# Performance work log

Measured on AMD Instinct MI355X. Metric: run time of the kernel, lower is better.

Reference implementation:

```python
import jax, jax.numpy as jnp
import numpy as np


def _gcn_conv(x, W, b, src, dst, num_nodes):
    # PyG GCNConv: h = x @ W; symmetric normalization with self-loops; scatter-add; + bias
    h = x @ W
    deg = jax.ops.segment_sum(jnp.ones_like(dst, dtype=h.dtype), dst, num_segments=num_nodes)
    dinv = jnp.where(deg > 0, jax.lax.rsqrt(deg), 0.0)
    norm = dinv[src] * dinv[dst]                         # [E]
    msgs = h[src] * norm[:, None]                        # [E, H] gather + scale
    out = jax.ops.segment_sum(msgs, dst, num_segments=num_nodes)
    return out + b


def setup_inputs() -> dict:
    key = jax.random.key(0)
    ks = jax.random.split(key, 10)
    N, E = 500000, 1000000
    IN, H, SIG = 3, 64, 24
    x = jax.random.uniform(ks[0], (N, IN), dtype=jnp.float32)
    edge_index = jax.random.randint(ks[1], (2, E), 0, N, dtype=jnp.int64)
    batch = jnp.zeros((N,), dtype=jnp.int64)
    def glorot(k, shape):
        lim = np.sqrt(6.0 / (shape[0] + shape[1]))
        return jax.random.uniform(k, shape, dtype=jnp.float32, minval=-lim, maxval=lim)
    return {
        "x": x,
        "edge_index": edge_index,
        "batch": batch,
        "W1": glorot(ks[2], (IN, H)), "b1": jnp.zeros((H,), jnp.float32),
        "W2": glorot(ks[3], (H, H)),  "b2": jnp.zeros((H,), jnp.float32),
        "W3": glorot(ks[4], (H, H)),  "b3": jnp.zeros((H,), jnp.float32),
        "Wfc": glorot(ks[5], (H, SIG)), "bfc": jnp.zeros((SIG,), jnp.float32),
    }


def reference(x, edge_index, batch, W1, b1, W2, b2, W3, b3, Wfc, bfc):
    N = x.shape[0]
    NUM_GRAPHS = 1  # batch is all zeros (single graph)
    # add self-loops once (GCNConv adds them per layer; identical edge set each layer)
    loop = jnp.arange(N, dtype=edge_index.dtype)
    src = jnp.concatenate([edge_index[0], loop])
    dst = jnp.concatenate([edge_index[1], loop])

    h = jax.nn.relu(_gcn_conv(x, W1, b1, src, dst, N))
    h = jax.nn.relu(_gcn_conv(h, W2, b2, src, dst, N))
    h = jax.nn.relu(_gcn_conv(h, W3, b3, src, dst, N))

    # global mean pool per graph
    sums = jax.ops.segment_sum(h, batch, num_segments=NUM_GRAPHS)          # [G, H]
    counts = jax.ops.segment_sum(jnp.ones((N,), h.dtype), batch, num_segments=NUM_GRAPHS)
    sig = sums / jnp.maximum(counts, 1.0)[:, None]

    return jnp.tanh(sig @ Wfc + bfc)  # [G, 24]
```

## Files before the change

kernel.cpp:

```cpp
#include <hip/hip_runtime.h>
#include <hip/hip_bf16.h>
#include <hip/hip_fp16.h>


#define ALIGN256(x) (((x) + 255) & ~(size_t)255)
#define NBUCK_MAX 512

typedef _Float16 half8 __attribute__((ext_vector_type(8)));
typedef _Float16 half4 __attribute__((ext_vector_type(4)));
typedef float f32x4 __attribute__((ext_vector_type(4)));
typedef int i32x4 __attribute__((ext_vector_type(4)));

__device__ __forceinline__ void dec16(i32x4 r, half8& a, half8& b) {
    i32x4 u, v;
    u.x = (int)(((unsigned)r.x << 8) & 0xFF00FF00u);
    u.y = (int)(((unsigned)r.x)      & 0xFF00FF00u);
    u.z = (int)(((unsigned)r.y << 8) & 0xFF00FF00u);
    u.w = (int)(((unsigned)r.y)      & 0xFF00FF00u);
    v.x = (int)(((unsigned)r.z << 8) & 0xFF00FF00u);
    v.y = (int)(((unsigned)r.z)      & 0xFF00FF00u);
    v.z = (int)(((unsigned)r.w << 8) & 0xFF00FF00u);
    v.w = (int)(((unsigned)r.w)      & 0xFF00FF00u);
    a = *(half8*)&u; b = *(half8*)&v;
}

__device__ __forceinline__ unsigned char enc8(float x) {
    unsigned short hb = __half_as_ushort(__float2half(x));
    return (unsigned char)((hb + 0x80u) >> 8);
}

__global__ __launch_bounds__(256) void init_kernel(float* __restrict__ pool, half4* __restrict__ xs,
                                                   unsigned char* __restrict__ h8a,
                                                   unsigned char* __restrict__ h8b, int N) {
    int i = threadIdx.x;
    if (i < 64) pool[i] = 0.f;
    if (i < 16) {
        ((int*)(h8a + (size_t)N * 64))[i] = 0;
        ((int*)(h8b + (size_t)N * 64))[i] = 0;
    }
    if (i == 0) *(int2*)&xs[N] = make_int2(0, 0);
}

__global__ __launch_bounds__(256) void hist_kernel(const int* __restrict__ ei, int E, int CE, int SH,
                                                   int* __restrict__ cnt_mat) {
    __shared__ int h[NBUCK_MAX];
    const int t = threadIdx.x, blk = blockIdx.x;
    for (int i = t; i < NBUCK_MAX; i += 256) h[i] = 0;
    __syncthreads();
    const int e0 = blk * CE, e1 = min(E, e0 + CE);
    for (int e = e0 + t; e < e1; e += 256)
        atomicAdd(&h[ei[E + e] >> SH], 1);
    __syncthreads();
    for (int i = t; i < NBUCK_MAX; i += 256) cnt_mat[blk * NBUCK_MAX + i] = h[i];
}

__global__ __launch_bounds__(64) void colscan_kernel(const int* __restrict__ cnt_mat,
                                                     int* __restrict__ base_mat,
                                                     int* __restrict__ tot, int nblk) {
    __shared__ int ls[64];
    const int j = blockIdx.x;
    const int t = threadIdx.x;
    const int PER = (nblk + 63) >> 6;
    const int b0 = t * PER, b1 = min(nblk, b0 + PER);
    int s = 0;
    for (int b = b0; b < b1; ++b) s += cnt_mat[b * NBUCK_MAX + j];
    ls[t] = s;
    __syncthreads();
    if (t == 0) {
        int run = 0;
        for (int k = 0; k < 64; ++k) { int v = ls[k]; ls[k] = run; run += v; }
        tot[j] = run;
    }
    __syncthreads();
    int run = ls[t];
    for (int b = b0; b < b1; ++b) {
        int v = cnt_mat[b * NBUCK_MAX + j];
        base_mat[b * NBUCK_MAX + j] = run;
        run += v;
    }
}

__global__ __launch_bounds__(256) void totscan_kernel(const int* __restrict__ tot,
                                                      int* __restrict__ start, int NBK) {
    __shared__ int ls[256];
    const int t = threadIdx.x;
    const int PER = (NBK + 255) >> 8;
    const int j0 = t * PER, j1 = min(NBK, j0 + PER);
    int s = 0;
    for (int j = j0; j < j1; ++j) s += tot[j];
    ls[t] = s;
    __syncthreads();
    if (t == 0) {
        int run = 0;
        for (int k = 0; k < 256; ++k) { int v = ls[k]; ls[k] = run; run += v; }
    }
    __syncthreads();
    int run = ls[t];
    for (int j = j0; j < j1; ++j) { start[j] = run; run += tot[j]; }
}

__global__ __launch_bounds__(256) void scatter_kernel(const int* __restrict__ ei, int E, int CE, int SH,
                                                      const int* __restrict__ base_mat,
                                                      const int* __restrict__ start,
                                                      unsigned* __restrict__ bkt) {
    __shared__ int sbuf[4096];
    __shared__ unsigned short sb[4096];
    __shared__ int lh[NBUCK_MAX];
    __shared__ int lbase[NBUCK_MAX];
    __shared__ int cur[NBUCK_MAX];
    __shared__ int ls[256];
    const int t = threadIdx.x, blk = blockIdx.x;
    for (int i = t; i < NBUCK_MAX; i += 256) { lh[i] = 0; cur[i] = 0; }
    __syncthreads();
    const int e0 = blk * CE, e1 = min(E, e0 + CE);
    for (int e = e0 + t; e < e1; e += 256)
        atomicAdd(&lh[ei[E + e] >> SH], 1);
    __syncthreads();
    int a0 = lh[2 * t], a1 = lh[2 * t + 1];
    ls[t] = a0 + a1;
    __syncthreads();
    if (t == 0) {
        int run = 0;
        for (int k = 0; k < 256; ++k) { int v = ls[k]; ls[k] = run; run += v; }
    }
    __syncthreads();
    lbase[2 * t]     = ls[t];
    lbase[2 * t + 1] = ls[t] + a0;
    __syncthreads();
    const unsigned lowm = (1u << SH) - 1u;
    for (int e = e0 + t; e < e1; e += 256) {
        int s = ei[e], d = ei[E + e];
        int b = d >> SH;
        int r = atomicAdd(&cur[b], 1);
        int slot = lbase[b] + r;
        sbuf[slot] = (int)((((unsigned)d & lowm) << 21) | (unsigned)s);
        sb[slot] = (unsigned short)b;
    }
    __syncthreads();
    const int n = e1 - e0;
    for (int i = t; i < n; i += 256) {
        int b = sb[i];
        int dest = start[b] + base_mat[blk * NBUCK_MAX + b] + (i - lbase[b]);
        bkt[dest] = (unsigned)sbuf[i];
    }
}

__global__ __launch_bounds__(256) void build_kernel(const unsigned* __restrict__ bkt,
                                                    const int* __restrict__ start, const int* __restrict__ tot,
                                                    int SH, int nrows,
                                                    int* __restrict__ ell, int* __restrict__ sec) {
    __shared__ __align__(16) int loc[2048][8];
    const int t = threadIdx.x, j = blockIdx.x;
    const int R = 1 << SH;
    int4 z = make_int4(0, 0, 0, 0);
    for (int i = t; i < R * 2; i += 256) ((int4*)loc)[i] = z;
    __syncthreads();
    const int s0 = start[j], s1 = s0 + tot[j];
    for (int e = s0 + t; e < s1; e += 256) {
        unsigned p = bkt[e];
        int dl = (int)(p >> 21);
        int src = (int)(p & 0x1FFFFFu);
        int k = atomicAdd(&loc[dl][0], 1);
        if (k < 7) loc[dl][1 + k] = src;
        else if (k < 15) {
            int grow = (j << SH) + dl;
            sec[(size_t)grow * 8 + (k - 7)] = src;
        }
    }
    __syncthreads();
    const int base = j << SH;
    for (int i = t; i < R; i += 256) {
        int grow = base + i;
        if (grow < nrows) {
            int4* dst = (int4*)(ell + (size_t)grow * 8);
            dst[0] = ((int4*)&loc[i][0])[0];
            dst[1] = ((int4*)&loc[i][0])[1];
        }
    }
}

__global__ __launch_bounds__(256) void xs_kernel(const int* __restrict__ ell, const float* __restrict__ x,
                                                 half4* __restrict__ xs, int N) {
    int i = blockIdx.x * 256 + threadIdx.x;
    if (i < N) {
        float d = rsqrtf((float)(ell[(size_t)i * 8] + 1));
        half4 v;
        v[0] = (_Float16)(d * x[(size_t)i * 3 + 0]);
        v[1] = (_Float16)(d * x[(size_t)i * 3 + 1]);
        v[2] = (_Float16)(d * x[(size_t)i * 3 + 2]);
        v[3] = (_Float16)0.f;
        xs[i] = v;
    }
}

__global__ __launch_bounds__(256) void layer1_kernel(const half4* __restrict__ xs,
                                                     const int* __restrict__ ell,
                                                     const int* __restrict__ sec,
                                                     const float* __restrict__ W1, const float* __restrict__ b1,
                                                     unsigned char* __restrict__ hout, int N) {
    __shared__ float4 a1S[256];
    const int t = threadIdx.x;
    const int jg = blockIdx.x * 256 + t;
    const bool valid = (jg < N);
    const int jc = valid ? jg : N;

    half4 sv = xs[jc];
    float sx = (float)sv[0], sy = (float)sv[1], sz = (float)sv[2];
    const int* row = ell + (size_t)(valid ? jg : 0) * 8;
    int4 e0 = *(const int4*)row;
    int4 e1 = *(const int4*)(row + 4);
    int craw = valid ? e0.x : 0;
    int deg = min(craw, 15);
    int i0 = (deg > 0) ? e0.y : N;
    int i1 = (deg > 1) ? e0.z : N;
    int i2 = (deg > 2) ? e0.w : N;
    int i3 = (deg > 3) ? e1.x : N;
    int i4 = (deg > 4) ? e1.y : N;
    int i5 = (deg > 5) ? e1.z : N;
    int i6 = (deg > 6) ? e1.w : N;
    half4 q0 = xs[i0], q1 = xs[i1], q2 = xs[i2], q3 = xs[i3];
    half4 q4 = xs[i4], q5 = xs[i5], q6 = xs[i6];
    sx += (float)q0[0] + (float)q1[0] + (float)q2[0] + (float)q3[0]
        + (float)q4[0] + (float)q5[0] + (float)q6[0];
    sy += (float)q0[1] + (float)q1[1] + (float)q2[1] + (float)q3[1]
        + (float)q4[1] + (float)q5[1] + (float)q6[1];
    sz += (float)q0[2] + (float)q1[2] + (float)q2[2] + (float)q3[2]
        + (float)q4[2] + (float)q5[2] + (float)q6[2];
    if (deg > 7) {
        const int* srow = sec + (size_t)jg * 8;
        for (int i = 7; i < deg; ++i) {
            half4 qq = xs[srow[i - 7]];
            sx += (float)qq[0]; sy += (float)qq[1]; sz += (float)qq[2];
        }
    }
    float dj = valid ? rsqrtf((float)(craw + 1)) : 0.f;
    a1S[t] = make_float4(dj * sx, dj * sy, dj * sz, dj);
    __syncthreads();

    const int l = t & 63, w = t >> 6;
    const float w0 = W1[l], w1 = W1[64 + l], w2 = W1[128 + l], bl = b1[l];
    const int base = blockIdx.x * 256 + w * 64;
    #pragma unroll 4
    for (int n = 0; n < 64; ++n) {
        int j2 = base + n;
        if (j2 >= N) break;
        float4 a = a1S[w * 64 + n];
        float v = fmaf(a.x, w0, fmaf(a.y, w1, fmaf(a.z, w2, bl)));
        hout[(size_t)j2 * 64 + l] = enc8(a.w * fmaxf(v, 0.f));
    }
}

template <int POOL>
__global__ __launch_bounds__(256) void layer_kernel(const unsigned char* __restrict__ hin,
                                                    const int* __restrict__ ell,
                                                    const int* __restrict__ sec,
                                                    const float* __restrict__ W, const float* __restrict__ bias,
                                                    unsigned char* __restrict__ hout, float* __restrict__ pool, int N) {
    const int t = threadIdx.x;
    const int l = t & 63;
    const int w = t >> 6;
    const int l15 = l & 15, q = l >> 4;
    const int m = l >> 2, qq = l & 3;
    const int cbase = l & ~3;

    __shared__ float red[256];
    __shared__ __align__(16) _Float16 wlds[8 * 64 * 8];
    __shared__ __align__(16) int tbuf[4][16 * 36];

    for (int c = t; c < 512; c += 256) {
        int f = c >> 6, ln = c & 63;
        int ct = f >> 1, kt = f & 1;
        int q2 = ln >> 4, m2 = ln & 15;
        half8 b;
        #pragma unroll
        for (int j = 0; j < 8; ++j) {
            int g = 4 * q2 + (j >> 1);
            int ii = g & 7, blk = g >> 3;
            int feat = 16 * blk + 4 * (ii >> 1) + (ii & 1) + 2 * (j & 1);
            b[j] = (_Float16)W[(kt * 32 + feat) * 64 + ct * 16 + m2];
        }
        *(half8*)&wlds[(size_t)c * 8] = b;
    }
    float bb[4];
    #pragma unroll
    for (int ct = 0; ct < 4; ++ct) bb[ct] = bias[ct * 16 + l15];
    __syncthreads();

    const char* hb = (const char*)hin;
    const int vlo = qq * 16;
    float ps0 = 0.f, ps1 = 0.f, ps2 = 0.f, ps3 = 0.f;

    const int ngroups = (N + 15) >> 4;
    const int gstride = gridDim.x * 4;
    for (int g = blockIdx.x * 4 + w; g < ngroups; g += gstride) {
        const int j0 = g << 4;
        const int jm = j0 + m;
        const bool validm = (jm < N);
        const int jsm = validm ? jm : N;

        i32x4 iv = *(const i32x4*)(ell + (size_t)jsm * 8 + (qq & 1) * 4);

        int cnt = __shfl(iv.x, cbase, 64);
        int s1  = __shfl(iv.y, cbase, 64);
        int s2  = __shfl(iv.z, cbase, 64);
        int s3  = __shfl(iv.w, cbase, 64);
        int s4  = __shfl(iv.x, cbase + 1, 64);
        int s5  = __shfl(iv.y, cbase + 1, 64);
        int s6  = __shfl(iv.z, cbase + 1, 64);
        int s7  = __shfl(iv.w, cbase + 1, 64);

        int craw = validm ? cnt : 0;
        int degc = min(craw, 15);
        float djv = rsqrtf((float)(craw + 1));

        int dmax = degc;
        dmax = max(dmax, __shfl_xor(dmax, 4, 64));
        dmax = max(dmax, __shfl_xor(dmax, 8, 64));
        dmax = max(dmax, __shfl_xor(dmax, 16, 64));
        dmax = max(dmax, __shfl_xor(dmax, 32, 64));

        s1 = (degc > 0) ? s1 : N;
        s2 = (degc > 1) ? s2 : N;
        s3 = (degc > 2) ? s3 : N;
        s4 = (degc > 3) ? s4 : N;
        s5 = (degc > 4) ? s5 : N;
        s6 = (degc > 5) ? s6 : N;
        s7 = (degc > 6) ? s7 : N;

        i32x4 rS = *(const i32x4*)(hb + ((size_t)jsm << 6) + vlo);
        i32x4 r1 = *(const i32x4*)(hb + ((size_t)(unsigned)s1 << 6) + vlo);
        i32x4 r2 = *(const i32x4*)(hb + ((size_t)(unsigned)s2 << 6) + vlo);
        i32x4 r3 = *(const i32x4*)(hb + ((size_t)(unsigned)s3 << 6) + vlo);
        i32x4 r4 = *(const i32x4*)(hb + ((size_t)(unsigned)s4 << 6) + vlo);
        const bool big = (dmax > 4);
        i32x4 r5, r6, r7;
        if (big) {
            r5 = *(const i32x4*)(hb + ((size_t)(unsigned)s5 << 6) + vlo);
            r6 = *(const i32x4*)(hb + ((size_t)(unsigned)s6 << 6) + vlo);
            r7 = *(const i32x4*)(hb + ((size_t)(unsigned)s7 << 6) + vlo);
        }

        half8 aA, aB, tA, tB;
        dec16(rS, aA, aB);
        dec16(r1, tA, tB); aA += tA; aB += tB;
        dec16(r2, tA, tB); aA += tA; aB += tB;
        dec16(r3, tA, tB); aA += tA; aB += tB;
        dec16(r4, tA, tB); aA += tA; aB += tB;
        if (big) {
            dec16(r5, tA, tB); aA += tA; aB += tB;
            dec16(r6, tA, tB); aA += tA; aB += tB;
            dec16(r7, tA, tB); aA += tA; aB += tB;
        }
        if (dmax > 7) {
            const int* srow = sec + (size_t)jsm * 8;
            #pragma unroll
            for (int ww = 8; ww < 16; ++ww) {
                int sr = (degc > ww - 1) ? srow[ww - 8] : N;
                i32x4 rt = *(const i32x4*)(hb + ((size_t)(unsigned)sr << 6) + vlo);
                dec16(rt, tA, tB); aA += tA; aB += tB;
            }
        }

        *(i32x4*)&tbuf[w][m * 36 + qq * 8]     = *(i32x4*)&aA;
        *(i32x4*)&tbuf[w][m * 36 + qq * 8 + 4] = *(i32x4*)&aB;
        half8 af0 = *(half8*)&tbuf[w][l15 * 36 + 4 * q];
        half8 af1 = *(half8*)&tbuf[w][l15 * 36 + 16 + 4 * q];

        const half8* wl = (const half8*)wlds;
        f32x4 c0 = {0.f, 0.f, 0.f, 0.f}, c1 = c0, c2 = c0, c3 = c0;
        c0 = __builtin_amdgcn_mfma_f32_16x16x32_f16(af0, wl[      l], c0, 0, 0, 0);
        c1 = __builtin_amdgcn_mfma_f32_16x16x32_f16(af0, wl[128 + l], c1, 0, 0, 0);
        c2 = __builtin_amdgcn_mfma_f32_16x16x32_f16(af0, wl[256 + l], c2, 0, 0, 0);
        c3 = __builtin_amdgcn_mfma_f32_16x16x32_f16(af0, wl[384 + l], c3, 0, 0, 0);
        c0 = __builtin_amdgcn_mfma_f32_16x16x32_f16(af1, wl[ 64 + l], c0, 0, 0, 0);
        c1 = __builtin_amdgcn_mfma_f32_16x16x32_f16(af1, wl[192 + l], c1, 0, 0, 0);
        c2 = __builtin_amdgcn_mfma_f32_16x16x32_f16(af1, wl[320 + l], c2, 0, 0, 0);
        c3 = __builtin_amdgcn_mfma_f32_16x16x32_f16(af1, wl[448 + l], c3, 0, 0, 0);

        if (POOL) {
            #pragma unroll
            for (int r = 0; r < 4; ++r) {
                int row = q * 4 + r;
                int gj = j0 + row;
                float djr = __shfl(djv, row << 2, 64);
                if (gj < N) {
                    ps0 += fmaxf(djr * c0[r] + bb[0], 0.f);
                    ps1 += fmaxf(djr * c1[r] + bb[1], 0.f);
                    ps2 += fmaxf(djr * c2[r] + bb[2], 0.f);
                    ps3 += fmaxf(djr * c3[r] + bb[3], 0.f);
                }
            }
        } else {
            #pragma unroll
            for (int r = 0; r < 4; ++r) {
                int row = q * 4 + r;
                int gj = j0 + row;
                float djr = __shfl(djv, row << 2, 64);
                if (gj < N) {
                    unsigned char* hp = hout + (size_t)gj * 64 + l15;
                    hp[0]  = enc8(djr * fmaxf(djr * c0[r] + bb[0], 0.f));
                    hp[16] = enc8(djr * fmaxf(djr * c1[r] + bb[1], 0.f));
                    hp[32] = enc8(djr * fmaxf(djr * c2[r] + bb[2], 0.f));
                    hp[48] = enc8(djr * fmaxf(djr * c3[r] + bb[3], 0.f));
                }
            }
        }
    }

    if (POOL) {
        ps0 += __shfl_xor(ps0, 16, 64); ps0 += __shfl_xor(ps0, 32, 64);
        ps1 += __shfl_xor(ps1, 16, 64); ps1 += __shfl_xor(ps1, 32, 64);
        ps2 += __shfl_xor(ps2, 16, 64); ps2 += __shfl_xor(ps2, 32, 64);
        ps3 += __shfl_xor(ps3, 16, 64); ps3 += __shfl_xor(ps3, 32, 64);
        if (q == 0) {
            red[w * 64 + l15]      = ps0;
            red[w * 64 + 16 + l15] = ps1;
            red[w * 64 + 32 + l15] = ps2;
            red[w * 64 + 48 + l15] = ps3;
        }
        __syncthreads();
        if (t < 64) {
            float s = red[t] + red[64 + t] + red[128 + t] + red[192 + t];
            atomicAdd(&pool[t], s);
        }
    }
}

__global__ __launch_bounds__(64) void final_kernel(const float* __restrict__ pool, const float* __restrict__ Wfc,
                                                   const float* __restrict__ bfc, float* __restrict__ out, int N) {
    int t = threadIdx.x;
    if (t < 24) {
        float inv = 1.0f / (float)N;
        float s = bfc[t];
        for (int c = 0; c < 64; ++c) s += pool[c] * inv * Wfc[c * 24 + t];
        out[t] = tanhf(s);
    }
}

extern "C" void kernel_launch(void* const* d_in, const int* in_sizes, int n_in,
                              void* d_out, int out_size, void* d_ws, size_t ws_size,
                              hipStream_t stream) {
    const float* x   = (const float*)d_in[0];
    const int*   ei  = (const int*)d_in[1];
    const float* W1  = (const float*)d_in[3];
    const float* b1  = (const float*)d_in[4];
    const float* W2  = (const float*)d_in[5];
    const float* b2  = (const float*)d_in[6];
    const float* W3  = (const float*)d_in[7];
    const float* b3  = (const float*)d_in[8];
    const float* Wfc = (const float*)d_in[9];
    const float* bfc = (const float*)d_in[10];
    float* out = (float*)d_out;

    const int N = in_sizes[2];
    const int E = in_sizes[1] / 2;

    size_t off = 0;
    auto take = [&](size_t bytes) -> char* {
        char* p = (char*)d_ws + off;
        off = ALIGN256(off + bytes);
        return p;
    };
    const int nrows = N + 16;
    int SH = 11;
    while ((((nrows - 1) >> SH) + 1) > NBUCK_MAX) ++SH;
    const int NBK = ((nrows - 1) >> SH) + 1;
    const int NCHUNK = (E + 4095) / 4096;
    const int CE = (E + NCHUNK - 1) / NCHUNK;

    int*           ell     = (int*)     take((size_t)nrows * 8 * 4);
    int*           sec     = (int*)     take((size_t)nrows * 8 * 4);
    unsigned*      bkt     = (unsigned*)take((size_t)E * 4);
    int*           cnt_mat = (int*)     take((size_t)NBUCK_MAX * NBUCK_MAX * 4);
    int*           base_mat= (int*)     take((size_t)NBUCK_MAX * NBUCK_MAX * 4);
    int*           tot     = (int*)     take(NBUCK_MAX * 4);
    int*           startb  = (int*)     take(NBUCK_MAX * 4);
    float*         pool    = (float*)   take(64 * 4);
    half4*         xs      = (half4*)   take(((size_t)N + 1) * 8);
    unsigned char* h8a     = (unsigned char*)take((size_t)(N + 1) * 64);
    unsigned char* h8b     = (unsigned char*)take((size_t)(N + 1) * 64);
    (void)ws_size; (void)n_in; (void)out_size;

    init_kernel<<<1, 256, 0, stream>>>(pool, xs, h8a, h8b, N);

    hist_kernel   <<<NCHUNK, 256, 0, stream>>>(ei, E, CE, SH, cnt_mat);
    colscan_kernel<<<NBK,     64, 0, stream>>>(cnt_mat, base_mat, tot, NCHUNK);
    totscan_kernel<<<1,      256, 0, stream>>>(tot, startb, NBK);
    scatter_kernel<<<NCHUNK, 256, 0, stream>>>(ei, E, CE, SH, base_mat, startb, bkt);
    build_kernel  <<<NBK,    256, 0, stream>>>(bkt, startb, tot, SH, nrows, ell, sec);

    xs_kernel<<<(N + 255) / 256, 256, 0, stream>>>(ell, x, xs, N);

    layer1_kernel<<<(N + 255) / 256, 256, 0, stream>>>(xs, ell, sec, W1, b1, h8a, N);

    int LB = 1024;
    const int ngroups = (N + 15) >> 4;
    const int maxb = (ngroups + 3) / 4;
    if (LB > maxb) LB = maxb;

    layer_kernel<0><<<LB, 256, 0, stream>>>(h8a, ell, sec, W2, b2, h8b, nullptr, N);

    layer_kernel<1><<<LB, 256, 0, stream>>>(h8b, ell, sec, W3, b3, nullptr, pool, N);

    final_kernel<<<1, 64, 0, stream>>>(pool, Wfc, bfc, out, N);
}
```

Baseline: 232.7 us.

## Fuse init, scans, xs prep and final head into neighboring kernels

Removes four small launches. The init work moves into hist_kernel block 0, the two scan kernels merge into a single-block scan, xs computation moves into build_kernel using shared-memory degrees, and the final FC+tanh runs in the last layer block via an atomic done counter. The aim is to cut launch and serialization overhead between tiny kernels. The price is that the merged scan is serial per bucket over all chunks in a single block, and the last-block pattern relies on fences for correctness.

```diff
diff --git a/kernel.cpp b/kernel.cpp
--- a/kernel.cpp
+++ b/kernel.cpp
@@ -29,22 +29,22 @@
     return (unsigned char)((hb + 0x80u) >> 8);
 }
 
-__global__ __launch_bounds__(256) void init_kernel(float* __restrict__ pool, half4* __restrict__ xs,
+__global__ __launch_bounds__(256) void hist_kernel(const int* __restrict__ ei, int E, int CE, int SH,
+                                                   int* __restrict__ cnt_mat,
+                                                   float* __restrict__ pool,
                                                    unsigned char* __restrict__ h8a,
-                                                   unsigned char* __restrict__ h8b, int N) {
-    int i = threadIdx.x;
-    if (i < 64) pool[i] = 0.f;
-    if (i < 16) {
-        ((int*)(h8a + (size_t)N * 64))[i] = 0;
-        ((int*)(h8b + (size_t)N * 64))[i] = 0;
-    }
-    if (i == 0) *(int2*)&xs[N] = make_int2(0, 0);
-}
-
-__global__ __launch_bounds__(256) void hist_kernel(const int* __restrict__ ei, int E, int CE, int SH,
-                                                   int* __restrict__ cnt_mat) {
+                                                   unsigned char* __restrict__ h8b,
+                                                   unsigned* __restrict__ done, int N) {
     __shared__ int h[NBUCK_MAX];
     const int t = threadIdx.x, blk = blockIdx.x;
+    if (blk == 0) {
+        if (t < 64) pool[t] = 0.f;
+        if (t < 16) {
+            ((int*)(h8a + (size_t)N * 64))[t] = 0;
+            ((int*)(h8b + (size_t)N * 64))[t] = 0;
+        }
+        if (t == 0) *done = 0u;
+    }
     for (int i = t; i < NBUCK_MAX; i += 256) h[i] = 0;
     __syncthreads();
     const int e0 = blk * CE, e1 = min(E, e0 + CE);
@@ -54,49 +54,26 @@
     for (int i = t; i < NBUCK_MAX; i += 256) cnt_mat[blk * NBUCK_MAX + i] = h[i];
 }
 
-__global__ __launch_bounds__(64) void colscan_kernel(const int* __restrict__ cnt_mat,
-                                                     int* __restrict__ base_mat,
-                                                     int* __restrict__ tot, int nblk) {
-    __shared__ int ls[64];
-    const int j = blockIdx.x;
+__global__ __launch_bounds__(256) void scan_kernel(const int* __restrict__ cnt_mat,
+                                                   int* __restrict__ base_mat,
+                                                   int* __restrict__ startb, int nchunk, int NBK) {
+    __shared__ int tots[NBUCK_MAX];
     const int t = threadIdx.x;
-    const int PER = (nblk + 63) >> 6;
-    const int b0 = t * PER, b1 = min(nblk, b0 + PER);
-    int s = 0;
-    for (int b = b0; b < b1; ++b) s += cnt_mat[b * NBUCK_MAX + j];
-    ls[t] = s;
+    for (int j = t; j < NBK; j += 256) {
+        int run = 0;
+        for (int b = 0; b < nchunk; ++b) {
+            int v = cnt_mat[b * NBUCK_MAX + j];
+            base_mat[b * NBUCK_MAX + j] = run;
+            run += v;
+        }
+        tots[j] = run;
+    }
     __syncthreads();
     if (t == 0) {
         int run = 0;
-        for (int k = 0; k < 64; ++k) { int v = ls[k]; ls[k] = run; run += v; }
-        tot[j] = run;
-    }
-    __syncthreads();
-    int run = ls[t];
-    for (int b = b0; b < b1; ++b) {
-        int v = cnt_mat[b * NBUCK_MAX + j];
-        base_mat[b * NBUCK_MAX + j] = run;
-        run += v;
-    }
-}
-
-__global__ __launch_bounds__(256) void totscan_kernel(const int* __restrict__ tot,
-                                                      int* __restrict__ start, int NBK) {
-    __shared__ int ls[256];
-    const int t = threadIdx.x;
-    const int PER = (NBK + 255) >> 8;
-    const int j0 = t * PER, j1 = min(NBK, j0 + PER);
-    int s = 0;
-    for (int j = j0; j < j1; ++j) s += tot[j];
-    ls[t] = s;
-    __syncthreads();
-    if (t == 0) {
-        int run = 0;
-        for (int k = 0; k < 256; ++k) { int v = ls[k]; ls[k] = run; run += v; }
-    }
-    __syncthreads();
-    int run = ls[t];
-    for (int j = j0; j < j1; ++j) { start[j] = run; run += tot[j]; }
+        for (int j = 0; j < NBK; ++j) { int v = tots[j]; startb[j] = run; run += v; }
+        startb[NBK] = run;
+    }
 }
 
 __global__ __launch_bounds__(256) void scatter_kernel(const int* __restrict__ ei, int E, int CE, int SH,
@@ -146,16 +123,18 @@
 }
 
 __global__ __launch_bounds__(256) void build_kernel(const unsigned* __restrict__ bkt,
-                                                    const int* __restrict__ start, const int* __restrict__ tot,
-                                                    int SH, int nrows,
-                                                    int* __restrict__ ell, int* __restrict__ sec) {
+                                                    const int* __restrict__ start,
+                                                    int SH, int nrows, int N,
+                                                    const float* __restrict__ x,
+                                                    int* __restrict__ ell, int* __restrict__ sec,
+                                                    half4* __restrict__ xs) {
     __shared__ __align__(16) int loc[2048][8];
     const int t = threadIdx.x, j = blockIdx.x;
     const int R = 1 << SH;
     int4 z = make_int4(0, 0, 0, 0);
     for (int i = t; i < R * 2; i += 256) ((int4*)loc)[i] = z;
     __syncthreads();
-    const int s0 = start[j], s1 = s0 + tot[j];
+    const int s0 = start[j], s1 = start[j + 1];
     for (int e = s0 + t; e < s1; e += 256) {
         unsigned p = bkt[e];
         int dl = (int)(p >> 21);
@@ -175,21 +154,18 @@
             int4* dst = (int4*)(ell + (size_t)grow * 8);
             dst[0] = ((int4*)&loc[i][0])[0];
             dst[1] = ((int4*)&loc[i][0])[1];
-        }
-    }
-}
-
-__global__ __launch_bounds__(256) void xs_kernel(const int* __restrict__ ell, const float* __restrict__ x,
-                                                 half4* __restrict__ xs, int N) {
-    int i = blockIdx.x * 256 + threadIdx.x;
-    if (i < N) {
-        float d = rsqrtf((float)(ell[(size_t)i * 8] + 1));
-        half4 v;
-        v[0] = (_Float16)(d * x[(size_t)i * 3 + 0]);
-        v[1] = (_Float16)(d * x[(size_t)i * 3 + 1]);
-        v[2] = (_Float16)(d * x[(size_t)i * 3 + 2]);
-        v[3] = (_Float16)0.f;
-        xs[i] = v;
+            if (grow < N) {
+                float d = rsqrtf((float)(loc[i][0] + 1));
+                half4 v;
+                v[0] = (_Float16)(d * x[(size_t)grow * 3 + 0]);
+                v[1] = (_Float16)(d * x[(size_t)grow * 3 + 1]);
+                v[2] = (_Float16)(d * x[(size_t)grow * 3 + 2]);
+                v[3] = (_Float16)0.f;
+                xs[grow] = v;
+            } else if (grow == N) {
+                *(int2*)&xs[N] = make_int2(0, 0);
+            }
+        }
     }
 }
 
@@ -255,7 +231,10 @@
                                                     const int* __restrict__ ell,
                                                     const int* __restrict__ sec,
                                                     const float* __restrict__ W, const float* __restrict__ bias,
-                                                    unsigned char* __restrict__ hout, float* __restrict__ pool, int N) {
+                                                    unsigned char* __restrict__ hout, float* __restrict__ pool,
+                                                    const float* __restrict__ Wfc, const float* __restrict__ bfc,
+                                                    float* __restrict__ out, unsigned* __restrict__ done,
+                                                    int nblocks, int N) {
     const int t = threadIdx.x;
     const int l = t & 63;
     const int w = t >> 6;
@@ -423,17 +402,21 @@
             float s = red[t] + red[64 + t] + red[128 + t] + red[192 + t];
             atomicAdd(&pool[t], s);
         }
-    }
-}
-
-__global__ __launch_bounds__(64) void final_kernel(const float* __restrict__ pool, const float* __restrict__ Wfc,
-                                                   const float* __restrict__ bfc, float* __restrict__ out, int N) {
-    int t = threadIdx.x;
-    if (t < 24) {
-        float inv = 1.0f / (float)N;
-        float s = bfc[t];
-        for (int c = 0; c < 64; ++c) s += pool[c] * inv * Wfc[c * 24 + t];
-        out[t] = tanhf(s);
+        __shared__ int lastFlag;
+        __syncthreads();
+        if (t == 0) {
+            __threadfence();
+            unsigned v = atomicAdd(done, 1u);
+            lastFlag = (v == (unsigned)(nblocks - 1));
+            __threadfence();
+        }
+        __syncthreads();
+        if (lastFlag && t < 24) {
+            float inv = 1.0f / (float)N;
+            float s2 = bfc[t];
+            for (int c = 0; c < 64; ++c) s2 += pool[c] * inv * Wfc[c * 24 + t];
+            out[t] = tanhf(s2);
+        }
     }
 }
 
@@ -473,23 +456,18 @@
     unsigned*      bkt     = (unsigned*)take((size_t)E * 4);
     int*           cnt_mat = (int*)     take((size_t)NBUCK_MAX * NBUCK_MAX * 4);
     int*           base_mat= (int*)     take((size_t)NBUCK_MAX * NBUCK_MAX * 4);
-    int*           tot     = (int*)     take(NBUCK_MAX * 4);
-    int*           startb  = (int*)     take(NBUCK_MAX * 4);
+    int*           startb  = (int*)     take((NBUCK_MAX + 1) * 4);
+    unsigned*      done    = (unsigned*)take(256);
     float*         pool    = (float*)   take(64 * 4);
     half4*         xs      = (half4*)   take(((size_t)N + 1) * 8);
     unsigned char* h8a     = (unsigned char*)take((size_t)(N + 1) * 64);
     unsigned char* h8b     = (unsigned char*)take((size_t)(N + 1) * 64);
     (void)ws_size; (void)n_in; (void)out_size;
 
-    init_kernel<<<1, 256, 0, stream>>>(pool, xs, h8a, h8b, N);
-
-    hist_kernel   <<<NCHUNK, 256, 0, stream>>>(ei, E, CE, SH, cnt_mat);
-    colscan_kernel<<<NBK,     64, 0, stream>>>(cnt_mat, base_mat, tot, NCHUNK);
-    totscan_kernel<<<1,      256, 0, stream>>>(tot, startb, NBK);
+    hist_kernel<<<NCHUNK, 256, 0, stream>>>(ei, E, CE, SH, cnt_mat, pool, h8a, h8b, done, N);
+    scan_kernel<<<1, 256, 0, stream>>>(cnt_mat, base_mat, startb, NCHUNK, NBK);
     scatter_kernel<<<NCHUNK, 256, 0, stream>>>(ei, E, CE, SH, base_mat, startb, bkt);
-    build_kernel  <<<NBK,    256, 0, stream>>>(bkt, startb, tot, SH, nrows, ell, sec);
-
-    xs_kernel<<<(N + 255) / 256, 256, 0, stream>>>(ell, x, xs, N);
+    build_kernel<<<NBK, 256, 0, stream>>>(bkt, startb, SH, nrows, N, x, ell, sec, xs);
 
     layer1_kernel<<<(N + 255) / 256, 256, 0, stream>>>(xs, ell, sec, W1, b1, h8a, N);
 
@@ -498,9 +476,9 @@
     const int maxb = (ngroups + 3) / 4;
     if (LB > maxb) LB = maxb;
 
-    layer_kernel<0><<<LB, 256, 0, stream>>>(h8a, ell, sec, W2, b2, h8b, nullptr, N);
-
-    layer_kernel<1><<<LB, 256, 0, stream>>>(h8b, ell, sec, W3, b3, nullptr, pool, N);
-
-    final_kernel<<<1, 64, 0, stream>>>(pool, Wfc, bfc, out, N);
-}
+    layer_kernel<0><<<LB, 256, 0, stream>>>(h8a, ell, sec, W2, b2, h8b, nullptr,
+                                            nullptr, nullptr, nullptr, nullptr, LB, N);
+
+    layer_kernel<1><<<LB, 256, 0, stream>>>(h8b, ell, sec, W3, b3, nullptr, pool,
+                                            Wfc, bfc, out, done, LB, N);
+}
```

Measured after the change: 315.5 us. +35.6%, slower.
